# Performance work log

Hardware: AMD Instinct MI355X
Metric: run time of the kernel (lower is better)

The kernel has to match this reference:

```python
import jax, jax.numpy as jnp
import numpy as np

S, B, IN, H, OUT = 512, 64, 512, 1024, 512


def _glorot(key, shape, fan_in):
    bound = 1.0 / np.sqrt(fan_in)
    return jax.random.uniform(key, shape, jnp.float32, -bound, bound)


def setup_inputs() -> dict:
    key = jax.random.key(0)
    ks = jax.random.split(key, 16)
    inp = {"x": jax.random.normal(ks[0], (S, B, IN), jnp.float32)}
    # layer 0: input IN -> H ; layer 1: H -> H. Gates stacked [f,i,o,c] -> 4H rows.
    inp["l0_Wx"] = _glorot(ks[1], (4 * H, IN), IN)
    inp["l0_Uh"] = _glorot(ks[2], (4 * H, H), H)
    inp["l0_bx"] = _glorot(ks[3], (4 * H,), IN)
    inp["l0_bh"] = _glorot(ks[4], (4 * H,), H)
    inp["l1_Wx"] = _glorot(ks[5], (4 * H, H), H)
    inp["l1_Uh"] = _glorot(ks[6], (4 * H, H), H)
    inp["l1_bx"] = _glorot(ks[7], (4 * H,), H)
    inp["l1_bh"] = _glorot(ks[8], (4 * H,), H)
    inp["fc_W"] = _glorot(ks[9], (OUT, H), H)
    inp["fc_b"] = _glorot(ks[10], (OUT,), H)
    return inp


def lstm_layer(x, Wx, Uh, bx, bh):
    # Precompute input projections for all timesteps in one big GEMM
    # (same math as per-step input2{f,i,o,c} Linears).
    xp = jnp.einsum("sbi,gi->sbg", x, Wx) + bx  # [S,B,4H]
    h0 = jnp.zeros((x.shape[1], H), x.dtype)
    c0 = jnp.zeros((x.shape[1], H), x.dtype)

    def step(carry, xp_t):
        h, c = carry
        gates = xp_t + h @ Uh.T + bh  # [B,4H]
        f, i, o, g = jnp.split(gates, 4, axis=-1)
        f, i, o = jax.nn.sigmoid(f), jax.nn.sigmoid(i), jax.nn.sigmoid(o)
        c = f * c + i * jnp.tanh(g)
        h = o * jnp.tanh(c)
        return (h, c), h

    (_, _), outs = jax.lax.scan(step, (h0, c0), xp)
    return outs  # [S,B,H]


def reference(x, l0_Wx, l0_Uh, l0_bx, l0_bh, l1_Wx, l1_Uh, l1_bx, l1_bh, fc_W, fc_b):
    h = lstm_layer(x, l0_Wx, l0_Uh, l0_bx, l0_bh)
    # hidden_activation_function defaults to Identity between layers
    h = lstm_layer(h, l1_Wx, l1_Uh, l1_bx, l1_bh)
    out = jnp.einsum("sbh,oh->sbo", h, fc_W) + fc_b  # [S,B,OUT]
    return out
```

## Files before the change

kernel.cpp:

```cpp
#include <hip/hip_runtime.h>
#include <hip/hip_bf16.h>

#define SDIM 512
#define BDIM 64
#define INDIM 512
#define HDIM 1024
#define OUTDIM 512
#define NWG 256
#define THREADS 512
#define BH (BDIM * HDIM)

typedef __bf16 bfreg;
typedef bfreg bf16x8 __attribute__((ext_vector_type(8)));
typedef bfreg bf16x4 __attribute__((ext_vector_type(4)));
typedef float f32x4 __attribute__((ext_vector_type(4)));
typedef float f32x16 __attribute__((ext_vector_type(16)));

__device__ __forceinline__ float sigf(float x) { return 1.f / (1.f + __expf(-x)); }
__device__ __forceinline__ float tanhfast(float x) { return 1.f - 2.f / (__expf(2.f * x) + 1.f); }


__global__ void cvt_bf16(bfreg* __restrict__ dst, const float* __restrict__ src, int n4)
{
    for (int i = blockIdx.x * blockDim.x + threadIdx.x; i < n4; i += gridDim.x * blockDim.x) {
        const float4 v = *(const float4*)(src + (size_t)i * 4);
        bf16x4 o;
        o[0] = (bfreg)v.x; o[1] = (bfreg)v.y; o[2] = (bfreg)v.z; o[3] = (bfreg)v.w;
        *(bf16x4*)(dst + (size_t)i * 4) = o;
    }
}

__global__ void bias_combine(float* __restrict__ b0, const float* __restrict__ bx0,
                             const float* __restrict__ bh0,
                             float* __restrict__ b1, const float* __restrict__ bx1,
                             const float* __restrict__ bh1)
{
    int i = blockIdx.x * blockDim.x + threadIdx.x;
    if (i < 4 * HDIM) {
        b0[i] = bx0[i] + bh0[i];
        b1[i] = bx1[i] + bh1[i];
    }
}

__global__ void pack_x(bfreg* __restrict__ dst, const float* __restrict__ src)
{
    const int total = SDIM * (INDIM / 8) * BDIM;
    for (int idx = blockIdx.x * blockDim.x + threadIdx.x; idx < total;
         idx += gridDim.x * blockDim.x) {
        const int b = idx & (BDIM - 1);
        const int r = idx >> 6;
        const int kb = r & (INDIM / 8 - 1);
        const int t = r >> 6;
        const float* s = src + ((size_t)t * BDIM + b) * INDIM + kb * 8;
        bfreg* d = dst + (size_t)idx * 8;
        #pragma unroll
        for (int j = 0; j < 8; ++j) d[j] = (bfreg)s[j];
    }
}

__global__ void pack_w(bfreg* __restrict__ dst, const float* __restrict__ Wx,
                       const float* __restrict__ Uh, int K0, int KH)
{
    const int KST16 = (K0 + KH) / 16;
    const int total = 128 * KST16 * 64;
    for (int idx = blockIdx.x * blockDim.x + threadIdx.x; idx < total;
         idx += gridDim.x * blockDim.x) {
        const int lane = idx & 63;
        int rem = idx >> 6;
        const int ks = rem % KST16;
        const int wg = rem / KST16;
        const int rr = lane & 31;
        const int g = rr >> 3, uo = rr & 7;
        const int row = g * HDIM + wg * 8 + uo;
        const int k = ks * 16 + (lane >> 5) * 8;
        const float* s = (k < K0) ? Wx + (size_t)row * K0 + k
                                  : Uh + (size_t)row * KH + (k - K0);
        bfreg* d = dst + (size_t)idx * 8;
        #pragma unroll
        for (int j = 0; j < 8; ++j) d[j] = (bfreg)s[j];
    }
}


__device__ __forceinline__ void wait_gen(const unsigned* g)
{
    while (__hip_atomic_load(g, __ATOMIC_RELAXED, __HIP_MEMORY_SCOPE_AGENT) == 0u)
        __builtin_amdgcn_s_sleep(1);
}

__device__ __forceinline__ void lds_spin(int* r, int target)
{
    while (__hip_atomic_load(r, __ATOMIC_ACQUIRE, __HIP_MEMORY_SCOPE_WORKGROUP) < target)
        __builtin_amdgcn_s_sleep(1);
}

template<int LAYER>
__device__ __forceinline__ void scan_layer(
    const bfreg* __restrict__ Pw, const float* __restrict__ biasL,
    const bfreg* __restrict__ x_pk,
    bfreg* __restrict__ Hb0, bfreg* __restrict__ Hb1,
    unsigned* __restrict__ sub0, unsigned* __restrict__ sub1,
    unsigned* __restrict__ gen0, unsigned* __restrict__ gen1,
    const int rg, char* smem)
{
    constexpr int KST16 = LAYER ? 128 : 96;
    constexpr int ECNT = LAYER ? 16 : 8;
    constexpr int LCNT = 16;

    const int tid = threadIdx.x;
    const int l = tid & 63;
    const int wid = tid >> 6;
    const int m = wid & 1;
    const int kq = wid >> 1;

    bfreg* lW = (bfreg*)smem;
    float* gatebuf = (float*)(smem + 128 * 1024);
    float* cbuf = gatebuf + 2 * 32 * 68;
    float* lbias = cbuf + 8 * 68;
    int* ready = (int*)(lbias + 32);

    {
        const float4* wsrc = (const float4*)(Pw + (size_t)rg * ((size_t)KST16 * 512));
        float4* wdst = (float4*)lW;
        for (int i = tid; i < KST16 * 64; i += THREADS) wdst[i] = wsrc[i];
    }
    if (tid < 32) lbias[tid] = biasL[(tid >> 3) * HDIM + rg * 8 + (tid & 7)];
    if (tid < 3) ready[tid] = 0;
    for (int i = tid; i < 8 * 68; i += THREADS) cbuf[i] = 0.f;
    __syncthreads();

    const int rowA = m * 32 + (l & 31);
    const int k8 = l >> 5;
    const int rr = l & 31;
    const int boff = 4 * (l >> 5);

    unsigned* mysub = LAYER ? sub1 : sub0;
    unsigned* mygen = LAYER ? gen1 : gen0;
    bfreg* Hme = LAYER ? Hb1 : Hb0;
    int* done = ready + 2;

    for (int t = 0; t < SDIM; ++t) {
        f32x16 acc = {};
        bf16x8 ev[ECNT];
        bf16x8 av[LCNT];

        if (!LAYER) {
            const bfreg* s0 = x_pk + (size_t)t * (64 * BDIM * 8);
            #pragma unroll
            for (int i = 0; i < ECNT; ++i) {
                const int ks = kq + 4 * i;
                const int cb = ks * 2 + k8;
                ev[i] = *(const bf16x8*)(s0 + (size_t)cb * 512 + rowA * 8);
            }
            __builtin_amdgcn_sched_barrier(0);
            if (t > 0) {
                if (wid == 0) {
                    wait_gen(gen0 + (size_t)(t - 1) * 16);
                    __hip_atomic_store(&ready[0], t, __ATOMIC_RELEASE,
                                       __HIP_MEMORY_SCOPE_WORKGROUP);
                } else {
                    lds_spin(&ready[0], t);
                }
            }
            asm volatile("" ::: "memory");
            const bfreg* s1 = Hb0 + (size_t)t * BH;
            #pragma unroll
            for (int i = 0; i < LCNT; ++i) {
                const int ks = kq + 4 * (8 + i);
                const int cb = (ks - 32) * 2 + k8;
                av[i] = *(const bf16x8*)(s1 + (size_t)cb * 512 + rowA * 8);
            }
            __builtin_amdgcn_sched_barrier(0);
        } else {
            if (wid == 0) {
                wait_gen(gen0 + (size_t)t * 16);
                __hip_atomic_store(&ready[0], t + 1, __ATOMIC_RELEASE,
                                   __HIP_MEMORY_SCOPE_WORKGROUP);
            } else {
                lds_spin(&ready[0], t + 1);
            }
            asm volatile("" ::: "memory");
            const bfreg* s0 = Hb0 + (size_t)(t + 1) * BH;
            #pragma unroll
            for (int i = 0; i < LCNT; ++i) {
                const int ks = kq + 4 * i;
                const int cb = ks * 2 + k8;
                av[i] = *(const bf16x8*)(s0 + (size_t)cb * 512 + rowA * 8);
            }
            __builtin_amdgcn_sched_barrier(0);
            if (t > 0) {
                if (wid == 4) {
                    wait_gen(gen1 + (size_t)(t - 1) * 16);
                    __hip_atomic_store(&ready[1], t, __ATOMIC_RELEASE,
                                       __HIP_MEMORY_SCOPE_WORKGROUP);
                } else {
                    lds_spin(&ready[1], t);
                }
            }
            asm volatile("" ::: "memory");
            const bfreg* s1 = Hb1 + (size_t)t * BH;
            #pragma unroll
            for (int i = 0; i < ECNT; ++i) {
                const int ks = kq + 4 * (16 + i);
                const int cb = (ks - 64) * 2 + k8;
                ev[i] = *(const bf16x8*)(s1 + (size_t)cb * 512 + rowA * 8);
            }
            __builtin_amdgcn_sched_barrier(0);
        }

        if (!LAYER) {
            #pragma unroll
            for (int i = 0; i < ECNT; ++i) {
                const int ks = kq + 4 * i;
                const bf16x8 w = *(const bf16x8*)(lW + ((size_t)ks * 64 + l) * 8);
                acc = __builtin_amdgcn_mfma_f32_32x32x16_bf16(ev[i], w, acc, 0, 0, 0);
            }
            #pragma unroll
            for (int i = 0; i < LCNT; ++i) {
                const int ks = kq + 4 * (8 + i);
                const bf16x8 w = *(const bf16x8*)(lW + ((size_t)ks * 64 + l) * 8);
                acc = __builtin_amdgcn_mfma_f32_32x32x16_bf16(av[i], w, acc, 0, 0, 0);
            }
        } else {
            #pragma unroll
            for (int i = 0; i < LCNT; ++i) {
                const int ks = kq + 4 * i;
                const bf16x8 w = *(const bf16x8*)(lW + ((size_t)ks * 64 + l) * 8);
                acc = __builtin_amdgcn_mfma_f32_32x32x16_bf16(av[i], w, acc, 0, 0, 0);
            }
            #pragma unroll
            for (int i = 0; i < ECNT; ++i) {
                const int ks = kq + 4 * (16 + i);
                const bf16x8 w = *(const bf16x8*)(lW + ((size_t)ks * 64 + l) * 8);
                acc = __builtin_amdgcn_mfma_f32_32x32x16_bf16(ev[i], w, acc, 0, 0, 0);
            }
        }

        if (wid >= 4) {
            float* slot = gatebuf + (kq - 2) * (32 * 68);
            #pragma unroll
            for (int q = 0; q < 4; ++q) {
                f32x4 v = { acc[4 * q], acc[4 * q + 1], acc[4 * q + 2], acc[4 * q + 3] };
                *(f32x4*)(slot + rr * 68 + m * 32 + 8 * q + boff) = v;
            }
        }
        __syncthreads();
        if (wid < 4) {
            float* slot = gatebuf + kq * (32 * 68);
            #pragma unroll
            for (int q = 0; q < 4; ++q) {
                float* pp = slot + rr * 68 + m * 32 + 8 * q + boff;
                f32x4 v = *(f32x4*)pp;
                v[0] += acc[4 * q];     v[1] += acc[4 * q + 1];
                v[2] += acc[4 * q + 2]; v[3] += acc[4 * q + 3];
                *(f32x4*)pp = v;
            }
        }
        __syncthreads();

        {
            const int uo = tid & 7, b = tid >> 3;
            float* g0 = gatebuf;
            float* g1 = gatebuf + 32 * 68;
            const float fv = g0[uo * 68 + b]        + g1[uo * 68 + b]        + lbias[uo];
            const float iv = g0[(8 + uo) * 68 + b]  + g1[(8 + uo) * 68 + b]  + lbias[8 + uo];
            const float ov = g0[(16 + uo) * 68 + b] + g1[(16 + uo) * 68 + b] + lbias[16 + uo];
            const float gv = g0[(24 + uo) * 68 + b] + g1[(24 + uo) * 68 + b] + lbias[24 + uo];
            const float c = cbuf[uo * 68 + b];
            const float fg = sigf(fv), ig = sigf(iv), og = sigf(ov);
            const float gg = tanhfast(gv);
            const float cn = fg * c + ig * gg;
            cbuf[uo * 68 + b] = cn;
            const bfreg hv = (bfreg)(og * tanhfast(cn));
            unsigned short hs;
            __builtin_memcpy(&hs, &hv, 2);
            const unsigned hw = hs;
            bfreg* dp = Hme + (size_t)(t + 1) * BH + rg * 512 + tid;
            asm volatile("global_store_short %0, %1, off sc0 sc1"
                         :: "v"(dp), "v"(hw) : "memory");
            asm volatile("s_waitcnt vmcnt(0)" ::: "memory");
        }
        if (l == 0)
            __hip_atomic_fetch_add(done, 1, __ATOMIC_ACQ_REL,
                                   __HIP_MEMORY_SCOPE_WORKGROUP);
        if (wid == 1) {
            while (__hip_atomic_load(done, __ATOMIC_ACQUIRE,
                                     __HIP_MEMORY_SCOPE_WORKGROUP) < 8 * (t + 1))
                __builtin_amdgcn_s_sleep(1);
            if (l == 0)
                __hip_atomic_fetch_add(mysub + (size_t)t * 128 + (rg >> 4) * 16, 1u,
                                       __ATOMIC_RELAXED, __HIP_MEMORY_SCOPE_AGENT);
        }
        if (rg == 0 && wid == 2) {
            const unsigned* sc = mysub + (size_t)t * 128;
            while (true) {
                unsigned v = (l < 8)
                    ? __hip_atomic_load(sc + l * 16, __ATOMIC_RELAXED,
                                        __HIP_MEMORY_SCOPE_AGENT)
                    : 16u;
                if (__all(v >= 16u)) break;
                __builtin_amdgcn_s_sleep(1);
            }
            asm volatile("" ::: "memory");
            if (l == 0)
                __hip_atomic_store(mygen + (size_t)t * 16, 1u,
                                   __ATOMIC_RELEASE, __HIP_MEMORY_SCOPE_AGENT);
        }
    }
}

__global__ __launch_bounds__(THREADS, 2)
void lstm_scan(const bfreg* __restrict__ Pw0, const bfreg* __restrict__ Pw1,
               const float* __restrict__ bias0, const float* __restrict__ bias1,
               const bfreg* __restrict__ x_pk,
               bfreg* __restrict__ Hb0, bfreg* __restrict__ Hb1,
               unsigned* __restrict__ sub0, unsigned* __restrict__ sub1,
               unsigned* __restrict__ gen0, unsigned* __restrict__ gen1)
{
    extern __shared__ char smem[];
    const int wgid = blockIdx.x;
    const int rg = wgid >> 1;
    if (wgid & 1)
        scan_layer<1>(Pw1, bias1, x_pk, Hb0, Hb1, sub0, sub1, gen0, gen1, rg, smem);
    else
        scan_layer<0>(Pw0, bias0, x_pk, Hb0, Hb1, sub0, sub1, gen0, gen1, rg, smem);
}

__global__ void fc_gemm(const bfreg* __restrict__ Hb1, const bfreg* __restrict__ Wb,
                        const float* __restrict__ bias, float* __restrict__ out)
{
    const int lane = threadIdx.x & 63;
    const int wid = threadIdx.x >> 6;
    const int cl = lane & 15, kg = lane >> 4;
    const int mbase = blockIdx.y * 64 + (wid >> 1) * 32;
    const int nbase = blockIdx.x * 64 + (wid & 1) * 32;
    const int t = mbase >> 6;
    const int b0 = mbase & 63;
    const bfreg* pa0 = Hb1 + (size_t)(t + 1) * BH + (size_t)kg * 512 + (b0 + cl) * 8;
    const bfreg* pa1 = pa0 + 16 * 8;
    const bfreg* pb0 = Wb + (size_t)(nbase + cl) * HDIM + kg * 8;
    const bfreg* pb1 = pb0 + (size_t)16 * HDIM;
    f32x4 acc[2][2] = {};
    #pragma unroll 4
    for (int k = 0; k < HDIM; k += 32) {
        const size_t co = (size_t)(k >> 3) * 512;
        const bf16x8 av0 = *(const bf16x8*)(pa0 + co);
        const bf16x8 av1 = *(const bf16x8*)(pa1 + co);
        const bf16x8 bv0 = *(const bf16x8*)(pb0 + k);
        const bf16x8 bv1 = *(const bf16x8*)(pb1 + k);
        acc[0][0] = __builtin_amdgcn_mfma_f32_16x16x32_bf16(av0, bv0, acc[0][0], 0, 0, 0);
        acc[0][1] = __builtin_amdgcn_mfma_f32_16x16x32_bf16(av0, bv1, acc[0][1], 0, 0, 0);
        acc[1][0] = __builtin_amdgcn_mfma_f32_16x16x32_bf16(av1, bv0, acc[1][0], 0, 0, 0);
        acc[1][1] = __builtin_amdgcn_mfma_f32_16x16x32_bf16(av1, bv1, acc[1][1], 0, 0, 0);
    }
    #pragma unroll
    for (int mi = 0; mi < 2; ++mi)
        #pragma unroll
        for (int ni = 0; ni < 2; ++ni)
            #pragma unroll
            for (int r = 0; r < 4; ++r) {
                const int row = mbase + mi * 16 + kg * 4 + r;
                const int col = nbase + ni * 16 + cl;
                out[(size_t)row * OUTDIM + col] = acc[mi][ni][r] + bias[col];
            }
}

extern "C" void kernel_launch(void* const* d_in, const int* in_sizes, int n_in,
                              void* d_out, int out_size, void* d_ws, size_t ws_size,
                              hipStream_t stream)
{
    const float* x     = (const float*)d_in[0];
    const float* l0_Wx = (const float*)d_in[1];
    const float* l0_Uh = (const float*)d_in[2];
    const float* l0_bx = (const float*)d_in[3];
    const float* l0_bh = (const float*)d_in[4];
    const float* l1_Wx = (const float*)d_in[5];
    const float* l1_Uh = (const float*)d_in[6];
    const float* l1_bx = (const float*)d_in[7];
    const float* l1_bh = (const float*)d_in[8];
    const float* fc_W  = (const float*)d_in[9];
    const float* fc_b  = (const float*)d_in[10];
    (void)in_sizes; (void)n_in; (void)out_size; (void)ws_size;

    char* p = (char*)d_ws;
    size_t off = 0;
    auto take = [&](size_t bytes) {
        void* r = p + off;
        off = (off + bytes + 255) & ~(size_t)255;
        return r;
    };

    bfreg* x_pk  = (bfreg*)take((size_t)SDIM * BDIM * INDIM * 2);
    bfreg* Pw0   = (bfreg*)take((size_t)128 * 96 * 512 * 2);
    bfreg* Pw1   = (bfreg*)take((size_t)128 * 128 * 512 * 2);
    bfreg* fcWb  = (bfreg*)take((size_t)OUTDIM * HDIM * 2);
    float* bias0 = (float*)take((size_t)4 * HDIM * 4);
    float* bias1 = (float*)take((size_t)4 * HDIM * 4);
    bfreg* Hb0   = (bfreg*)take((size_t)(SDIM + 1) * BH * 2);
    bfreg* Hb1   = (bfreg*)take((size_t)(SDIM + 1) * BH * 2);
    unsigned* sub0 = (unsigned*)take((size_t)SDIM * 128 * 4);
    unsigned* sub1 = (unsigned*)take((size_t)SDIM * 128 * 4);
    unsigned* gen0 = (unsigned*)take((size_t)SDIM * 16 * 4);
    unsigned* gen1 = (unsigned*)take((size_t)SDIM * 16 * 4);

    hipMemsetAsync(Hb0, 0, (size_t)BH * 2, stream);
    hipMemsetAsync(Hb1, 0, (size_t)BH * 2, stream);
    hipMemsetAsync(sub0, 0, (size_t)SDIM * 128 * 4, stream);
    hipMemsetAsync(sub1, 0, (size_t)SDIM * 128 * 4, stream);
    hipMemsetAsync(gen0, 0, (size_t)SDIM * 16 * 4, stream);
    hipMemsetAsync(gen1, 0, (size_t)SDIM * 16 * 4, stream);

    pack_x<<<4096, 256, 0, stream>>>(x_pk, x);
    cvt_bf16<<<512, 256, 0, stream>>>(fcWb, fc_W, OUTDIM * HDIM / 4);
    pack_w<<<3072, 256, 0, stream>>>(Pw0, l0_Wx, l0_Uh, INDIM, HDIM);
    pack_w<<<4096, 256, 0, stream>>>(Pw1, l1_Wx, l1_Uh, HDIM, HDIM);
    bias_combine<<<16, 256, 0, stream>>>(bias0, l0_bx, l0_bh, bias1, l1_bx, l1_bh);

    const int smem_bytes = 128 * 1024 + 2 * 32 * 68 * 4 + 8 * 68 * 4 + 32 * 4 + 16;
    hipFuncSetAttribute((const void*)lstm_scan,
                        hipFuncAttributeMaxDynamicSharedMemorySize, smem_bytes);
    lstm_scan<<<NWG, THREADS, smem_bytes, stream>>>(Pw0, Pw1, bias0, bias1,
                                                    x_pk, Hb0, Hb1,
                                                    sub0, sub1, gen0, gen1);

    fc_gemm<<<dim3(OUTDIM / 64, SDIM * BDIM / 64), 256, 0, stream>>>(
        Hb1, fcWb, fc_b, (float*)d_out);
}
```

Baseline: 2.726 ms.

## Replace global generation flags with per-wave partial sub-counter waits

The two-level barrier is removed. Before, one workgroup aggregated the sub-counters into a generation flag and one wave per workgroup relayed it through LDS. Now each wave polls only the two sub-counters covering the contiguous K-slice of H it is about to read. The K-step assignment per wave changes from interleaved to contiguous so that each wave depends on only 2 of the 8 producer groups. This is meant to remove the extra hop through the aggregator and the LDS relay from the per-timestep critical path. In exchange, many more waves poll global atomics.

```diff
diff --git a/kernel.cpp b/kernel.cpp
--- a/kernel.cpp
+++ b/kernel.cpp
@@ -82,16 +82,15 @@
 }
 
 
-__device__ __forceinline__ void wait_gen(const unsigned* g)
-{
-    while (__hip_atomic_load(g, __ATOMIC_RELAXED, __HIP_MEMORY_SCOPE_AGENT) == 0u)
+__device__ __forceinline__ void wait_sub2(const unsigned* base, int l)
+{
+    const unsigned* p = base + (l & 1) * 16;
+    const bool act = (l < 2);
+    while (true) {
+        unsigned v = __hip_atomic_load(p, __ATOMIC_RELAXED, __HIP_MEMORY_SCOPE_AGENT);
+        if (__all(!act || v >= 16u)) break;
         __builtin_amdgcn_s_sleep(1);
-}
-
-__device__ __forceinline__ void lds_spin(int* r, int target)
-{
-    while (__hip_atomic_load(r, __ATOMIC_ACQUIRE, __HIP_MEMORY_SCOPE_WORKGROUP) < target)
-        __builtin_amdgcn_s_sleep(1);
+    }
 }
 
 template<int LAYER>
@@ -100,7 +99,6 @@
     const bfreg* __restrict__ x_pk,
     bfreg* __restrict__ Hb0, bfreg* __restrict__ Hb1,
     unsigned* __restrict__ sub0, unsigned* __restrict__ sub1,
-    unsigned* __restrict__ gen0, unsigned* __restrict__ gen1,
     const int rg, char* smem)
 {
     constexpr int KST16 = LAYER ? 128 : 96;
@@ -117,7 +115,7 @@
     float* gatebuf = (float*)(smem + 128 * 1024);
     float* cbuf = gatebuf + 2 * 32 * 68;
     float* lbias = cbuf + 8 * 68;
-    int* ready = (int*)(lbias + 32);
+    int* done = (int*)(lbias + 32);
 
     {
         const float4* wsrc = (const float4*)(Pw + (size_t)rg * ((size_t)KST16 * 512));
@@ -125,7 +123,7 @@
         for (int i = tid; i < KST16 * 64; i += THREADS) wdst[i] = wsrc[i];
     }
     if (tid < 32) lbias[tid] = biasL[(tid >> 3) * HDIM + rg * 8 + (tid & 7)];
-    if (tid < 3) ready[tid] = 0;
+    if (tid == 0) *done = 0;
     for (int i = tid; i < 8 * 68; i += THREADS) cbuf[i] = 0.f;
     __syncthreads();
 
@@ -135,9 +133,7 @@
     const int boff = 4 * (l >> 5);
 
     unsigned* mysub = LAYER ? sub1 : sub0;
-    unsigned* mygen = LAYER ? gen1 : gen0;
     bfreg* Hme = LAYER ? Hb1 : Hb0;
-    int* done = ready + 2;
 
     for (int t = 0; t < SDIM; ++t) {
         f32x16 acc = {};
@@ -148,60 +144,40 @@
             const bfreg* s0 = x_pk + (size_t)t * (64 * BDIM * 8);
             #pragma unroll
             for (int i = 0; i < ECNT; ++i) {
-                const int ks = kq + 4 * i;
+                const int ks = kq * 8 + i;
                 const int cb = ks * 2 + k8;
                 ev[i] = *(const bf16x8*)(s0 + (size_t)cb * 512 + rowA * 8);
             }
             __builtin_amdgcn_sched_barrier(0);
-            if (t > 0) {
-                if (wid == 0) {
-                    wait_gen(gen0 + (size_t)(t - 1) * 16);
-                    __hip_atomic_store(&ready[0], t, __ATOMIC_RELEASE,
-                                       __HIP_MEMORY_SCOPE_WORKGROUP);
-                } else {
-                    lds_spin(&ready[0], t);
-                }
-            }
+            if (t > 0)
+                wait_sub2(sub0 + (size_t)(t - 1) * 128 + 2 * kq * 16, l);
             asm volatile("" ::: "memory");
             const bfreg* s1 = Hb0 + (size_t)t * BH;
             #pragma unroll
             for (int i = 0; i < LCNT; ++i) {
-                const int ks = kq + 4 * (8 + i);
+                const int ks = 32 + kq * 16 + i;
                 const int cb = (ks - 32) * 2 + k8;
                 av[i] = *(const bf16x8*)(s1 + (size_t)cb * 512 + rowA * 8);
             }
             __builtin_amdgcn_sched_barrier(0);
         } else {
-            if (wid == 0) {
-                wait_gen(gen0 + (size_t)t * 16);
-                __hip_atomic_store(&ready[0], t + 1, __ATOMIC_RELEASE,
-                                   __HIP_MEMORY_SCOPE_WORKGROUP);
-            } else {
-                lds_spin(&ready[0], t + 1);
-            }
+            wait_sub2(sub0 + (size_t)t * 128 + 2 * kq * 16, l);
             asm volatile("" ::: "memory");
             const bfreg* s0 = Hb0 + (size_t)(t + 1) * BH;
             #pragma unroll
             for (int i = 0; i < LCNT; ++i) {
-                const int ks = kq + 4 * i;
+                const int ks = kq * 16 + i;
                 const int cb = ks * 2 + k8;
                 av[i] = *(const bf16x8*)(s0 + (size_t)cb * 512 + rowA * 8);
             }
             __builtin_amdgcn_sched_barrier(0);
-            if (t > 0) {
-                if (wid == 4) {
-                    wait_gen(gen1 + (size_t)(t - 1) * 16);
-                    __hip_atomic_store(&ready[1], t, __ATOMIC_RELEASE,
-                                       __HIP_MEMORY_SCOPE_WORKGROUP);
-                } else {
-                    lds_spin(&ready[1], t);
-                }
-            }
+            if (t > 0)
+                wait_sub2(sub1 + (size_t)(t - 1) * 128 + 2 * kq * 16, l);
             asm volatile("" ::: "memory");
             const bfreg* s1 = Hb1 + (size_t)t * BH;
             #pragma unroll
             for (int i = 0; i < ECNT; ++i) {
-                const int ks = kq + 4 * (16 + i);
+                const int ks = 64 + kq * 16 + i;
                 const int cb = (ks - 64) * 2 + k8;
                 ev[i] = *(const bf16x8*)(s1 + (size_t)cb * 512 + rowA * 8);
             }
@@ -211,26 +187,26 @@
         if (!LAYER) {
             #pragma unroll
             for (int i = 0; i < ECNT; ++i) {
-                const int ks = kq + 4 * i;
+                const int ks = kq * 8 + i;
                 const bf16x8 w = *(const bf16x8*)(lW + ((size_t)ks * 64 + l) * 8);
                 acc = __builtin_amdgcn_mfma_f32_32x32x16_bf16(ev[i], w, acc, 0, 0, 0);
             }
             #pragma unroll
             for (int i = 0; i < LCNT; ++i) {
-                const int ks = kq + 4 * (8 + i);
+                const int ks = 32 + kq * 16 + i;
                 const bf16x8 w = *(const bf16x8*)(lW + ((size_t)ks * 64 + l) * 8);
                 acc = __builtin_amdgcn_mfma_f32_32x32x16_bf16(av[i], w, acc, 0, 0, 0);
             }
         } else {
             #pragma unroll
             for (int i = 0; i < LCNT; ++i) {
-                const int ks = kq + 4 * i;
+                const int ks = kq * 16 + i;
                 const bf16x8 w = *(const bf16x8*)(lW + ((size_t)ks * 64 + l) * 8);
                 acc = __builtin_amdgcn_mfma_f32_32x32x16_bf16(av[i], w, acc, 0, 0, 0);
             }
             #pragma unroll
             for (int i = 0; i < ECNT; ++i) {
-                const int ks = kq + 4 * (16 + i);
+                const int ks = 64 + kq * 16 + i;
                 const bf16x8 w = *(const bf16x8*)(lW + ((size_t)ks * 64 + l) * 8);
                 acc = __builtin_amdgcn_mfma_f32_32x32x16_bf16(ev[i], w, acc, 0, 0, 0);
             }
@@ -291,21 +267,6 @@
                 __hip_atomic_fetch_add(mysub + (size_t)t * 128 + (rg >> 4) * 16, 1u,
                                        __ATOMIC_RELAXED, __HIP_MEMORY_SCOPE_AGENT);
         }
-        if (rg == 0 && wid == 2) {
-            const unsigned* sc = mysub + (size_t)t * 128;
-            while (true) {
-                unsigned v = (l < 8)
-                    ? __hip_atomic_load(sc + l * 16, __ATOMIC_RELAXED,
-                                        __HIP_MEMORY_SCOPE_AGENT)
-                    : 16u;
-                if (__all(v >= 16u)) break;
-                __builtin_amdgcn_s_sleep(1);
-            }
-            asm volatile("" ::: "memory");
-            if (l == 0)
-                __hip_atomic_store(mygen + (size_t)t * 16, 1u,
-                                   __ATOMIC_RELEASE, __HIP_MEMORY_SCOPE_AGENT);
-        }
     }
 }
 
@@ -314,16 +275,15 @@
                const float* __restrict__ bias0, const float* __restrict__ bias1,
                const bfreg* __restrict__ x_pk,
                bfreg* __restrict__ Hb0, bfreg* __restrict__ Hb1,
-               unsigned* __restrict__ sub0, unsigned* __restrict__ sub1,
-               unsigned* __restrict__ gen0, unsigned* __restrict__ gen1)
+               unsigned* __restrict__ sub0, unsigned* __restrict__ sub1)
 {
     extern __shared__ char smem[];
     const int wgid = blockIdx.x;
     const int rg = wgid >> 1;
     if (wgid & 1)
-        scan_layer<1>(Pw1, bias1, x_pk, Hb0, Hb1, sub0, sub1, gen0, gen1, rg, smem);
+        scan_layer<1>(Pw1, bias1, x_pk, Hb0, Hb1, sub0, sub1, rg, smem);
     else
-        scan_layer<0>(Pw0, bias0, x_pk, Hb0, Hb1, sub0, sub1, gen0, gen1, rg, smem);
+        scan_layer<0>(Pw0, bias0, x_pk, Hb0, Hb1, sub0, sub1, rg, smem);
 }
 
 __global__ void fc_gemm(const bfreg* __restrict__ Hb1, const bfreg* __restrict__ Wb,
@@ -400,15 +360,11 @@
     bfreg* Hb1   = (bfreg*)take((size_t)(SDIM + 1) * BH * 2);
     unsigned* sub0 = (unsigned*)take((size_t)SDIM * 128 * 4);
     unsigned* sub1 = (unsigned*)take((size_t)SDIM * 128 * 4);
-    unsigned* gen0 = (unsigned*)take((size_t)SDIM * 16 * 4);
-    unsigned* gen1 = (unsigned*)take((size_t)SDIM * 16 * 4);
 
     hipMemsetAsync(Hb0, 0, (size_t)BH * 2, stream);
     hipMemsetAsync(Hb1, 0, (size_t)BH * 2, stream);
     hipMemsetAsync(sub0, 0, (size_t)SDIM * 128 * 4, stream);
     hipMemsetAsync(sub1, 0, (size_t)SDIM * 128 * 4, stream);
-    hipMemsetAsync(gen0, 0, (size_t)SDIM * 16 * 4, stream);
-    hipMemsetAsync(gen1, 0, (size_t)SDIM * 16 * 4, stream);
 
     pack_x<<<4096, 256, 0, stream>>>(x_pk, x);
     cvt_bf16<<<512, 256, 0, stream>>>(fcWb, fc_W, OUTDIM * HDIM / 4);
@@ -420,8 +376,7 @@
     hipFuncSetAttribute((const void*)lstm_scan,
                         hipFuncAttributeMaxDynamicSharedMemorySize, smem_bytes);
     lstm_scan<<<NWG, THREADS, smem_bytes, stream>>>(Pw0, Pw1, bias0, bias1,
-                                                    x_pk, Hb0, Hb1,
-                                                    sub0, sub1, gen0, gen1);
+                                                    x_pk, Hb0, Hb1, sub0, sub1);
 
     fc_gemm<<<dim3(OUTDIM / 64, SDIM * BDIM / 64), 256, 0, stream>>>(
         Hb1, fcWb, fc_b, (float*)d_out);
```

Result: slower. 4.576 ms (+67.9%).
